# Kernel optimization log

Measured on AMD Instinct MI355X. Metric: run time of the kernel, lower is better.

Reference implementation:

```python
import jax, jax.numpy as jnp
import numpy as np

PAD_IDX_WORD = 0
EOS_IDX = 3
BOT_IDX = 1
B, S, T = 64, 1024, 128
VOCAB = 30000


def setup_inputs() -> dict:
    key = jax.random.key(0)
    k1, k2, k3 = jax.random.split(key, 3)
    W = jax.random.randint(k1, (B, S), 0, VOCAB)                 # token ids (for pad/eos mask)
    emissions = jax.random.normal(k2, (B, S, T), dtype=jnp.float32)  # per-token tag scores (BOS stripped)
    transitions = jax.random.uniform(k3, (T, T), minval=-0.1, maxval=0.1, dtype=jnp.float32)
    return {"W": W, "emissions": emissions, "transitions": transitions}


def reference(W, emissions, transitions):
    """Linear-chain CRF log-partition (normalizer) via backward DP, batched.

    Faithful to NeuralCRF.normalizer: for n = nw-2 .. 0:
        addends[b,i,j] = transitions[i,j] + emissions[b,n+1,j] + Beta[b,j]
        Beta[b,i]      = logsumexp_j(addends) where mask[b,n+1] else Beta[b,i]
    logZ[b] = logsumexp_i(transitions[bot,i] + emissions[b,0,i] + Beta[b,i])
    """
    mask = ~((W == PAD_IDX_WORD) | (W == EOS_IDX))                # [B, S]
    # steps consume emissions[:, n+1] for n = S-2 .. 0  ->  reversed emissions[:, 1:]
    em_rev = jnp.flip(emissions[:, 1:, :], axis=1).transpose(1, 0, 2)  # [S-1, B, T]
    m_rev = jnp.flip(mask[:, 1:], axis=1).T                            # [S-1, B]
    Beta0 = jnp.zeros((W.shape[0], transitions.shape[0]), dtype=emissions.dtype)

    def step(Beta, xs):
        em_n, m_n = xs                                            # [B,T], [B]
        addends = transitions[None, :, :] + em_n[:, None, :] + Beta[:, None, :]  # [B,T,T]
        osum = jax.nn.logsumexp(addends, axis=2)                  # [B,T]
        return jnp.where(m_n[:, None], osum, Beta), None

    Beta, _ = jax.lax.scan(step, Beta0, (em_rev, m_rev))
    final = transitions[BOT_IDX, :][None, :] + emissions[:, 0, :] + Beta  # [B,T]
    return jax.nn.logsumexp(final, axis=1)                        # [B] logZ
```

## Files before the change

### kernel.cpp

```cpp
#include <hip/hip_runtime.h>


typedef _Float16 h8 __attribute__((ext_vector_type(8)));
typedef float    f4 __attribute__((ext_vector_type(4)));

#define B_  64
#define S_  1024
#define T_  128
#define G_  16
#define PAD_IDX 0
#define EOS_IDX 3
#define BOT_IDX 1
#define GHAT         5.35f
#define EXP_NEG_GHAT 0.004736892f

__device__ __forceinline__ int baddr16(int n, int k_slot ) {
  return n * 256 + (((k_slot ^ n) & 15) << 4);
}

__global__ __launch_bounds__(256)
void crf_seg_kernel(const int* __restrict__ W,
                    const float* __restrict__ emissions,
                    const float* __restrict__ transitions,
                    _Float16* __restrict__ ws)
{
  const int b = blockIdx.x, g = blockIdx.y;
  const int tid  = threadIdx.x;
  const int w    = tid >> 6;
  const int lane = tid & 63;
  const int lr   = lane & 15;
  const int lg   = lane >> 4;

  __shared__ __align__(16) char bbuf[2][32768];

  int tok = W[b * S_ + g * 64 + lane];
  unsigned long long mask = __ballot((tok != PAD_IDX) & (tok != EOS_IDX));
  if (g == 0) mask &= ~1ull;

  const size_t segoff = ((size_t)(b * G_ + g)) << 14;

  if (mask == 0ull) {
    int r = tid >> 1, c0 = (tid & 1) << 6;
    #pragma unroll
    for (int e8 = 0; e8 < 8; ++e8) {
      h8 v;
      #pragma unroll
      for (int e = 0; e < 8; ++e)
        v[e] = (r == c0 + e8 * 8 + e) ? (_Float16)1.f : (_Float16)0.f;
      *(h8*)(ws + segoff + (size_t)r * T_ + c0 + e8 * 8) = v;
    }
    return;
  }

  h8 EA[2][4];
  #pragma unroll
  for (int rtl = 0; rtl < 2; ++rtl) {
    const int row = 32 * w + 16 * rtl + lr;
    #pragma unroll
    for (int kb = 0; kb < 4; ++kb) {
      const float4* tp = (const float4*)(transitions + (size_t)row * T_ + kb * 32 + lg * 8);
      float4 v0 = tp[0], v1 = tp[1];
      h8 f;
      f[0] = (_Float16)(__expf(v0.x) * EXP_NEG_GHAT);
      f[1] = (_Float16)(__expf(v0.y) * EXP_NEG_GHAT);
      f[2] = (_Float16)(__expf(v0.z) * EXP_NEG_GHAT);
      f[3] = (_Float16)(__expf(v0.w) * EXP_NEG_GHAT);
      f[4] = (_Float16)(__expf(v1.x) * EXP_NEG_GHAT);
      f[5] = (_Float16)(__expf(v1.y) * EXP_NEG_GHAT);
      f[6] = (_Float16)(__expf(v1.z) * EXP_NEG_GHAT);
      f[7] = (_Float16)(__expf(v1.w) * EXP_NEG_GHAT);
      EA[rtl][kb] = f;
    }
  }

  const int hib = 63 - __builtin_clzll(mask);
  {
    char* bz = &bbuf[0][0] + tid * 128;
    #pragma unroll
    for (int r = 0; r < 8; ++r) *(uint4*)(bz + r * 16) = uint4{0u, 0u, 0u, 0u};
  }
  __syncthreads();
  if (tid < T_) {
    float e = emissions[((size_t)b * S_ + (g * 64 + hib)) * T_ + tid];
    *(_Float16*)(&bbuf[0][baddr16(tid, tid >> 3) + (tid & 7) * 2]) = (_Float16)__expf(e);
  }

  unsigned long long rem = mask & ~(1ull << hib);
  int inb = rem ? (63 - __builtin_clzll(rem)) : -1;
  const int base_r = 32 * w + lg * 4;
  float4 elo, ehi;
  {
    int idx = (inb < 0) ? 0 : (g * 64 + inb);
    const float* ep = emissions + ((size_t)b * S_ + idx) * T_;
    elo = *(const float4*)(ep + base_r);
    ehi = *(const float4*)(ep + base_r + 16);
  }

  int p = 0;
  f4 acc[2][8];
  for (;;) {
    __syncthreads();

    #pragma unroll
    for (int rtl = 0; rtl < 2; ++rtl)
      #pragma unroll
      for (int ct = 0; ct < 8; ++ct) acc[rtl][ct] = f4{0.f, 0.f, 0.f, 0.f};

    #pragma unroll
    for (int kb = 0; kb < 4; ++kb) {
      #pragma unroll
      for (int ct = 0; ct < 8; ++ct) {
        const int n = ct * 16 + lr;
        h8 bf = *(const h8*)(&bbuf[p][baddr16(n, kb * 4 + lg)]);
        acc[0][ct] = __builtin_amdgcn_mfma_f32_16x16x32_f16(EA[0][kb], bf, acc[0][ct], 0, 0, 0);
        acc[1][ct] = __builtin_amdgcn_mfma_f32_16x16x32_f16(EA[1][kb], bf, acc[1][ct], 0, 0, 0);
      }
    }

    if (inb < 0) break;

    f4 ulo, uhi;
    ulo[0] = __expf(elo.x); ulo[1] = __expf(elo.y);
    ulo[2] = __expf(elo.z); ulo[3] = __expf(elo.w);
    uhi[0] = __expf(ehi.x); uhi[1] = __expf(ehi.y);
    uhi[2] = __expf(ehi.z); uhi[3] = __expf(ehi.w);

    rem &= ~(1ull << inb);
    int inn = rem ? (63 - __builtin_clzll(rem)) : -1;
    {
      int idx = (inn < 0) ? 0 : (g * 64 + inn);
      const float* ep = emissions + ((size_t)b * S_ + idx) * T_;
      elo = *(const float4*)(ep + base_r);
      ehi = *(const float4*)(ep + base_r + 16);
    }

    #pragma unroll
    for (int rtl = 0; rtl < 2; ++rtl) {
      const int k0 = 32 * w + 16 * rtl + lg * 4;
      const int ks = k0 >> 3;
      const int sub = (k0 & 7) * 2;
      const f4 u = rtl ? uhi : ulo;
      #pragma unroll
      for (int ct = 0; ct < 8; ++ct) {
        const int n = ct * 16 + lr;
        f4 c = acc[rtl][ct];
        uint2 d;
        d.x = __builtin_bit_cast(unsigned,
                __builtin_amdgcn_cvt_pkrtz(c[0] * u[0], c[1] * u[1]));
        d.y = __builtin_bit_cast(unsigned,
                __builtin_amdgcn_cvt_pkrtz(c[2] * u[2], c[3] * u[3]));
        *(uint2*)(&bbuf[p ^ 1][baddr16(n, ks) + sub]) = d;
      }
    }
    p ^= 1;
    inb = inn;
  }

  #pragma unroll
  for (int rtl = 0; rtl < 2; ++rtl) {
    const int k0 = 32 * w + 16 * rtl + lg * 4;
    #pragma unroll
    for (int ct = 0; ct < 8; ++ct) {
      const int n = ct * 16 + lr;
      #pragma unroll
      for (int r = 0; r < 4; ++r)
        ws[segoff + (size_t)(k0 + r) * T_ + n] = (_Float16)acc[rtl][ct][r];
    }
  }
}

__global__ __launch_bounds__(128)
void crf_combine_kernel(const int* __restrict__ W,
                        const float* __restrict__ emissions,
                        const float* __restrict__ transitions,
                        const _Float16* __restrict__ ws,
                        float* __restrict__ out)
{
  const int b = blockIdx.x, t = threadIdx.x;
  __shared__ float qv[T_];
  __shared__ float redf[128];
  __shared__ int   redi[128];

  qv[t] = 1.0f;
  __syncthreads();

  for (int g = G_ - 1; g >= 0; --g) {
    const _Float16* Sg = ws + (((size_t)(b * G_ + g)) << 14) + (size_t)t * T_;
    float acc = 0.f;
    #pragma unroll
    for (int j8 = 0; j8 < 16; ++j8) {
      h8 v = *(const h8*)(Sg + j8 * 8);
      float4 q0 = *(const float4*)&qv[j8 * 8];
      float4 q1 = *(const float4*)&qv[j8 * 8 + 4];
      acc += (float)v[0] * q0.x + (float)v[1] * q0.y
           + (float)v[2] * q0.z + (float)v[3] * q0.w
           + (float)v[4] * q1.x + (float)v[5] * q1.y
           + (float)v[6] * q1.z + (float)v[7] * q1.w;
    }
    __syncthreads();
    qv[t] = acc;
    __syncthreads();
  }

  int cnt = 0;
  #pragma unroll
  for (int c = 0; c < 8; ++c) {
    int i = c * 128 + t;
    if (i >= 1) {
      int tk = W[b * S_ + i];
      cnt += ((tk != PAD_IDX) & (tk != EOS_IDX)) ? 1 : 0;
    }
  }

  float term = __expf(transitions[BOT_IDX * T_ + t]
                      + emissions[(size_t)b * S_ * T_ + t]) * qv[t];
  redf[t] = term;
  redi[t] = cnt;
  __syncthreads();
  #pragma unroll
  for (int off = 64; off > 0; off >>= 1) {
    if (t < off) { redf[t] += redf[t + off]; redi[t] += redi[t + off]; }
    __syncthreads();
  }
  if (t == 0) out[b] = GHAT * (float)redi[0] + logf(redf[0]);
}

extern "C" void kernel_launch(void* const* d_in, const int* in_sizes, int n_in,
                              void* d_out, int out_size, void* d_ws, size_t ws_size,
                              hipStream_t stream) {
  const int*   W     = (const int*)d_in[0];
  const float* em    = (const float*)d_in[1];
  const float* trans = (const float*)d_in[2];
  float*       out   = (float*)d_out;
  _Float16*    wsp   = (_Float16*)d_ws;
  (void)in_sizes; (void)n_in; (void)out_size; (void)ws_size;

  crf_seg_kernel<<<dim3(B_, G_), 256, 0, stream>>>(W, em, trans, wsp);
  crf_combine_kernel<<<B_, 128, 0, stream>>>(W, em, trans, wsp, out);
}
```

Baseline: 342.5 us.

## Split segment transfer-matrix columns across 8 blocks to raise parallelism

```diff
diff --git a/kernel.cpp b/kernel.cpp
--- a/kernel.cpp
+++ b/kernel.cpp
@@ -1,37 +1,40 @@
 #include <hip/hip_runtime.h>
 
 
-typedef _Float16 h8 __attribute__((ext_vector_type(8)));
-typedef float    f4 __attribute__((ext_vector_type(4)));
+typedef _Float16 h8  __attribute__((ext_vector_type(8)));
+typedef float    f4  __attribute__((ext_vector_type(4)));
+typedef unsigned u4v __attribute__((ext_vector_type(4)));
 
 #define B_  64
 #define S_  1024
 #define T_  128
 #define G_  16
+#define CS_ 8
+#define N_  16
 #define PAD_IDX 0
 #define EOS_IDX 3
 #define BOT_IDX 1
 #define GHAT         5.35f
 #define EXP_NEG_GHAT 0.004736892f
 
-__device__ __forceinline__ int baddr16(int n, int k_slot ) {
-  return n * 256 + (((k_slot ^ n) & 15) << 4);
-}
-
-__global__ __launch_bounds__(256)
+__device__ __forceinline__ int baddr16(int n, int ks) {
+  return n * 256 + (((ks ^ n) & 15) << 4);
+}
+
+__global__ __launch_bounds__(128)
 void crf_seg_kernel(const int* __restrict__ W,
                     const float* __restrict__ emissions,
                     const float* __restrict__ transitions,
                     _Float16* __restrict__ ws)
 {
-  const int b = blockIdx.x, g = blockIdx.y;
+  const int b = blockIdx.x, g = blockIdx.y, cs = blockIdx.z;
   const int tid  = threadIdx.x;
   const int w    = tid >> 6;
   const int lane = tid & 63;
   const int lr   = lane & 15;
   const int lg   = lane >> 4;
 
-  __shared__ __align__(16) char bbuf[2][32768];
+  __shared__ __align__(16) char bbuf[2][4096];
 
   int tok = W[b * S_ + g * 64 + lane];
   unsigned long long mask = __ballot((tok != PAD_IDX) & (tok != EOS_IDX));
@@ -40,132 +43,117 @@
   const size_t segoff = ((size_t)(b * G_ + g)) << 14;
 
   if (mask == 0ull) {
-    int r = tid >> 1, c0 = (tid & 1) << 6;
-    #pragma unroll
-    for (int e8 = 0; e8 < 8; ++e8) {
-      h8 v;
-      #pragma unroll
-      for (int e = 0; e < 8; ++e)
-        v[e] = (r == c0 + e8 * 8 + e) ? (_Float16)1.f : (_Float16)0.f;
-      *(h8*)(ws + segoff + (size_t)r * T_ + c0 + e8 * 8) = v;
-    }
+    _Float16 vals[16];
+    #pragma unroll
+    for (int e = 0; e < 16; ++e)
+      vals[e] = (tid == 16 * cs + e) ? (_Float16)1.f : (_Float16)0.f;
+    *(h8*)(ws + segoff + (size_t)tid * T_ + 16 * cs)     = *(h8*)&vals[0];
+    *(h8*)(ws + segoff + (size_t)tid * T_ + 16 * cs + 8) = *(h8*)&vals[8];
     return;
   }
 
-  h8 EA[2][4];
-  #pragma unroll
-  for (int rtl = 0; rtl < 2; ++rtl) {
-    const int row = 32 * w + 16 * rtl + lr;
+  u4v EA[4][4];
+  #pragma unroll
+  for (int rtl = 0; rtl < 4; ++rtl) {
+    const int row = 64 * w + 16 * rtl + lr;
     #pragma unroll
     for (int kb = 0; kb < 4; ++kb) {
       const float4* tp = (const float4*)(transitions + (size_t)row * T_ + kb * 32 + lg * 8);
-      float4 v0 = tp[0], v1 = tp[1];
+      float4 x = tp[0], y = tp[1];
       h8 f;
-      f[0] = (_Float16)(__expf(v0.x) * EXP_NEG_GHAT);
-      f[1] = (_Float16)(__expf(v0.y) * EXP_NEG_GHAT);
-      f[2] = (_Float16)(__expf(v0.z) * EXP_NEG_GHAT);
-      f[3] = (_Float16)(__expf(v0.w) * EXP_NEG_GHAT);
-      f[4] = (_Float16)(__expf(v1.x) * EXP_NEG_GHAT);
-      f[5] = (_Float16)(__expf(v1.y) * EXP_NEG_GHAT);
-      f[6] = (_Float16)(__expf(v1.z) * EXP_NEG_GHAT);
-      f[7] = (_Float16)(__expf(v1.w) * EXP_NEG_GHAT);
-      EA[rtl][kb] = f;
+      f[0] = (_Float16)(__expf(x.x) * EXP_NEG_GHAT);
+      f[1] = (_Float16)(__expf(x.y) * EXP_NEG_GHAT);
+      f[2] = (_Float16)(__expf(x.z) * EXP_NEG_GHAT);
+      f[3] = (_Float16)(__expf(x.w) * EXP_NEG_GHAT);
+      f[4] = (_Float16)(__expf(y.x) * EXP_NEG_GHAT);
+      f[5] = (_Float16)(__expf(y.y) * EXP_NEG_GHAT);
+      f[6] = (_Float16)(__expf(y.z) * EXP_NEG_GHAT);
+      f[7] = (_Float16)(__expf(y.w) * EXP_NEG_GHAT);
+      EA[rtl][kb] = __builtin_bit_cast(u4v, f);
     }
   }
 
   const int hib = 63 - __builtin_clzll(mask);
-  {
-    char* bz = &bbuf[0][0] + tid * 128;
-    #pragma unroll
-    for (int r = 0; r < 8; ++r) *(uint4*)(bz + r * 16) = uint4{0u, 0u, 0u, 0u};
-  }
+  *(uint4*)(&bbuf[0][tid * 32])      = uint4{0u, 0u, 0u, 0u};
+  *(uint4*)(&bbuf[0][tid * 32 + 16]) = uint4{0u, 0u, 0u, 0u};
   __syncthreads();
-  if (tid < T_) {
-    float e = emissions[((size_t)b * S_ + (g * 64 + hib)) * T_ + tid];
-    *(_Float16*)(&bbuf[0][baddr16(tid, tid >> 3) + (tid & 7) * 2]) = (_Float16)__expf(e);
+  if (tid < N_) {
+    int k = 16 * cs + tid;
+    float e = emissions[((size_t)b * S_ + (g * 64 + hib)) * T_ + k];
+    *(_Float16*)(&bbuf[0][baddr16(tid, k >> 3) + (k & 7) * 2]) = (_Float16)__expf(e);
   }
 
   unsigned long long rem = mask & ~(1ull << hib);
   int inb = rem ? (63 - __builtin_clzll(rem)) : -1;
-  const int base_r = 32 * w + lg * 4;
-  float4 elo, ehi;
+  float4 epf[4];
   {
     int idx = (inb < 0) ? 0 : (g * 64 + inb);
     const float* ep = emissions + ((size_t)b * S_ + idx) * T_;
-    elo = *(const float4*)(ep + base_r);
-    ehi = *(const float4*)(ep + base_r + 16);
+    #pragma unroll
+    for (int rtl = 0; rtl < 4; ++rtl)
+      epf[rtl] = *(const float4*)(ep + 64 * w + 16 * rtl + 4 * lg);
   }
 
   int p = 0;
-  f4 acc[2][8];
+  f4 acc[4];
   for (;;) {
-    __syncthreads();
-
-    #pragma unroll
-    for (int rtl = 0; rtl < 2; ++rtl)
+    #pragma unroll
+    for (int rtl = 0; rtl < 4; ++rtl)
       #pragma unroll
-      for (int ct = 0; ct < 8; ++ct) acc[rtl][ct] = f4{0.f, 0.f, 0.f, 0.f};
+      for (int kb = 0; kb < 4; ++kb)
+        asm volatile("" : "+v"(EA[rtl][kb]));
+
+    __syncthreads();
+
+    #pragma unroll
+    for (int rtl = 0; rtl < 4; ++rtl) acc[rtl] = f4{0.f, 0.f, 0.f, 0.f};
 
     #pragma unroll
     for (int kb = 0; kb < 4; ++kb) {
+      h8 bf = *(const h8*)(&bbuf[p][baddr16(lr, kb * 4 + lg)]);
       #pragma unroll
-      for (int ct = 0; ct < 8; ++ct) {
-        const int n = ct * 16 + lr;
-        h8 bf = *(const h8*)(&bbuf[p][baddr16(n, kb * 4 + lg)]);
-        acc[0][ct] = __builtin_amdgcn_mfma_f32_16x16x32_f16(EA[0][kb], bf, acc[0][ct], 0, 0, 0);
-        acc[1][ct] = __builtin_amdgcn_mfma_f32_16x16x32_f16(EA[1][kb], bf, acc[1][ct], 0, 0, 0);
-      }
+      for (int rtl = 0; rtl < 4; ++rtl)
+        acc[rtl] = __builtin_amdgcn_mfma_f32_16x16x32_f16(
+            __builtin_bit_cast(h8, EA[rtl][kb]), bf, acc[rtl], 0, 0, 0);
     }
 
     if (inb < 0) break;
-
-    f4 ulo, uhi;
-    ulo[0] = __expf(elo.x); ulo[1] = __expf(elo.y);
-    ulo[2] = __expf(elo.z); ulo[3] = __expf(elo.w);
-    uhi[0] = __expf(ehi.x); uhi[1] = __expf(ehi.y);
-    uhi[2] = __expf(ehi.z); uhi[3] = __expf(ehi.w);
 
     rem &= ~(1ull << inb);
     int inn = rem ? (63 - __builtin_clzll(rem)) : -1;
+    float4 ecur[4];
+    #pragma unroll
+    for (int rtl = 0; rtl < 4; ++rtl) ecur[rtl] = epf[rtl];
     {
       int idx = (inn < 0) ? 0 : (g * 64 + inn);
       const float* ep = emissions + ((size_t)b * S_ + idx) * T_;
-      elo = *(const float4*)(ep + base_r);
-      ehi = *(const float4*)(ep + base_r + 16);
-    }
-
-    #pragma unroll
-    for (int rtl = 0; rtl < 2; ++rtl) {
-      const int k0 = 32 * w + 16 * rtl + lg * 4;
-      const int ks = k0 >> 3;
-      const int sub = (k0 & 7) * 2;
-      const f4 u = rtl ? uhi : ulo;
       #pragma unroll
-      for (int ct = 0; ct < 8; ++ct) {
-        const int n = ct * 16 + lr;
-        f4 c = acc[rtl][ct];
-        uint2 d;
-        d.x = __builtin_bit_cast(unsigned,
-                __builtin_amdgcn_cvt_pkrtz(c[0] * u[0], c[1] * u[1]));
-        d.y = __builtin_bit_cast(unsigned,
-                __builtin_amdgcn_cvt_pkrtz(c[2] * u[2], c[3] * u[3]));
-        *(uint2*)(&bbuf[p ^ 1][baddr16(n, ks) + sub]) = d;
-      }
+      for (int rtl = 0; rtl < 4; ++rtl)
+        epf[rtl] = *(const float4*)(ep + 64 * w + 16 * rtl + 4 * lg);
+    }
+
+    #pragma unroll
+    for (int rtl = 0; rtl < 4; ++rtl) {
+      const int k0 = 64 * w + 16 * rtl + 4 * lg;
+      f4 c = acc[rtl];
+      float4 e = ecur[rtl];
+      uint2 d;
+      d.x = __builtin_bit_cast(unsigned,
+              __builtin_amdgcn_cvt_pkrtz(c[0] * __expf(e.x), c[1] * __expf(e.y)));
+      d.y = __builtin_bit_cast(unsigned,
+              __builtin_amdgcn_cvt_pkrtz(c[2] * __expf(e.z), c[3] * __expf(e.w)));
+      *(uint2*)(&bbuf[p ^ 1][baddr16(lr, k0 >> 3) + (k0 & 7) * 2]) = d;
     }
     p ^= 1;
     inb = inn;
   }
 
   #pragma unroll
-  for (int rtl = 0; rtl < 2; ++rtl) {
-    const int k0 = 32 * w + 16 * rtl + lg * 4;
-    #pragma unroll
-    for (int ct = 0; ct < 8; ++ct) {
-      const int n = ct * 16 + lr;
-      #pragma unroll
-      for (int r = 0; r < 4; ++r)
-        ws[segoff + (size_t)(k0 + r) * T_ + n] = (_Float16)acc[rtl][ct][r];
-    }
+  for (int rtl = 0; rtl < 4; ++rtl) {
+    const int k0 = 64 * w + 16 * rtl + 4 * lg;
+    #pragma unroll
+    for (int r = 0; r < 4; ++r)
+      ws[segoff + (size_t)(k0 + r) * T_ + 16 * cs + lr] = (_Float16)acc[rtl][r];
   }
 }
 
@@ -235,6 +223,6 @@
   _Float16*    wsp   = (_Float16*)d_ws;
   (void)in_sizes; (void)n_in; (void)out_size; (void)ws_size;
 
-  crf_seg_kernel<<<dim3(B_, G_), 256, 0, stream>>>(W, em, trans, wsp);
+  crf_seg_kernel<<<dim3(B_, G_, CS_), 128, 0, stream>>>(W, em, trans, wsp);
   crf_combine_kernel<<<B_, 128, 0, stream>>>(W, em, trans, wsp, out);
 }
```

Measured after the change: 496.2 us. 44.9% more time.
